# Performance work log

Measured on AMD Instinct MI355X. Metric: run time of the kernel, lower is better.

## Reference

```python
import jax, jax.numpy as jnp
import numpy as np

N = 50000   # nodes
E = 800000  # edges (avg degree 16)
D = 128     # in_feats == out_feats


def setup_inputs() -> dict:
    key = jax.random.key(0)
    k1, k2, k3, k4 = jax.random.split(key, 4)
    h = jax.random.normal(k1, (N, D), dtype=jnp.float32)
    src = jax.random.randint(k2, (E,), 0, N, dtype=jnp.int32)
    dst = jax.random.randint(k3, (E,), 0, N, dtype=jnp.int32)
    snorm_n = jnp.ones((N, 1), dtype=jnp.float32)  # sqrt(1/N) replicated; identity-scaled here
    # NodeApply linear: Linear(2*D, D) with bias
    W = jax.random.normal(k4, (D, 2 * D), dtype=jnp.float32) / np.sqrt(2 * D).astype(np.float32)
    b = jnp.zeros((D,), dtype=jnp.float32)
    return {"h": h, "snorm_n": snorm_n, "W": W, "b": b, "src": src, "dst": dst}


def reference(h, snorm_n, W, b, src, dst):
    # dropout p=0.0 -> identity
    h_in = h
    # gather neighbor messages and segment-mean aggregate (MeanAggregator)
    ones = jnp.ones((src.shape[0],), dtype=h.dtype)
    deg = jax.ops.segment_sum(ones, dst, num_segments=N)            # [N]
    msg_sum = jax.ops.segment_sum(h[src], dst, num_segments=N)     # [N, D]
    c = msg_sum / jnp.maximum(deg, 1.0)[:, None]                   # zero-degree nodes -> c = 0
    # NodeApply: concat -> linear -> L2 normalize -> relu
    bundle = jnp.concatenate([h, c], axis=1) @ W.T + b             # [N, D]
    nrm = jnp.sqrt(jnp.sum(bundle * bundle, axis=1, keepdims=True))
    bundle = bundle / jnp.maximum(nrm, 1e-12)                      # F.normalize(p=2, dim=1)
    out = jax.nn.relu(bundle)
    # graph norm
    out = out * snorm_n
    # residual (in_feats == out_feats)
    return h_in + out
```

## Files before the change

### kernel.cpp

```cpp
#include <hip/hip_runtime.h>
#include <hip/hip_bf16.h>

#define TPB 256
#define CHUNK_LOG 13
#define CHUNK (1 << CHUNK_LOG)
#define HSTRIDE 12544

typedef __attribute__((ext_vector_type(8))) short bf16x8;
typedef __attribute__((ext_vector_type(4))) float f32x4;

__device__ inline unsigned short f2bf(float f) {
    unsigned u = __float_as_uint(f);
    unsigned r = u + 0x7fffu + ((u >> 16) & 1u);
    return (unsigned short)(r >> 16);
}
__device__ inline float bf2f(unsigned short s) {
    return __uint_as_float(((unsigned)s) << 16);
}

__global__ void k_conv(const float* __restrict__ h, const float* __restrict__ W,
                       unsigned short* __restrict__ h_hi,
                       unsigned short* __restrict__ Wb, int N) {
    int t = blockIdx.x * TPB + threadIdx.x;
    int nh4 = N * 32;
    if (t < nh4) {
        float4 v = ((const float4*)h)[t];
        ushort4 hi;
        hi.x = f2bf(v.x); hi.y = f2bf(v.y);
        hi.z = f2bf(v.z); hi.w = f2bf(v.w);
        ((ushort4*)h_hi)[t] = hi;
    } else if (t - nh4 < 8192) {
        int w4 = t - nh4;
        float4 v = ((const float4*)W)[w4];
        ushort4 hi;
        hi.x = f2bf(v.x); hi.y = f2bf(v.y);
        hi.z = f2bf(v.z); hi.w = f2bf(v.w);
        ((ushort4*)Wb)[w4] = hi;
    }
}

__global__ void k_hist(const int* __restrict__ dst,
                       unsigned* __restrict__ hist32, unsigned char* __restrict__ lrank,
                       int E) {
    __shared__ unsigned lhist[HSTRIDE];
    int b = blockIdx.x;
    for (int i = threadIdx.x; i < HSTRIDE; i += TPB) lhist[i] = 0;
    __syncthreads();
    int e0 = b << CHUNK_LOG;
    int e1 = min(e0 + CHUNK, E);
    for (int e = e0 + (int)threadIdx.x; e < e1; e += TPB) {
        int d = dst[e];
        unsigned sh = (d & 3) * 8;
        unsigned old = atomicAdd(&lhist[d >> 2], 1u << sh);
        lrank[e] = (unsigned char)((old >> sh) & 0xffu);
    }
    __syncthreads();
    for (int i = threadIdx.x; i < HSTRIDE; i += TPB)
        hist32[(size_t)b * HSTRIDE + i] = lhist[i];
}

__global__ void k_colscan(const unsigned* __restrict__ hist32,
                          unsigned short* __restrict__ cbase, int* __restrict__ deg,
                          int* __restrict__ bsum, int N, int NBH) {
    extern __shared__ unsigned tile[];
    __shared__ int sdata[4];
    int tileBase = blockIdx.x * 64;
    int total = NBH * 64;
    for (int i = threadIdx.x; i < total; i += TPB) {
        int b = i >> 6, c = i & 63;
        tile[i] = hist32[(size_t)b * HSTRIDE + tileBase + c];
    }
    __syncthreads();
    int t = threadIdx.x;
    int n = blockIdx.x * TPB + t;
    unsigned sh = (t & 3) * 8;
    int wcol = t >> 2;
    int run = 0;
    for (int b = 0; b < NBH; ++b) {
        int c = (int)((tile[b * 64 + wcol] >> sh) & 0xffu);
        if (n < N) cbase[(size_t)b * N + n] = (unsigned short)run;
        run += c;
    }
    if (n < N) deg[n] = run; else run = 0;
    int s = run;
    for (int o = 32; o; o >>= 1) s += __shfl_xor(s, o);
    int lane = t & 63, w = t >> 6;
    if (lane == 0) sdata[w] = s;
    __syncthreads();
    if (t == 0) bsum[blockIdx.x] = sdata[0] + sdata[1] + sdata[2] + sdata[3];
}

__global__ void k_offs2(const int* __restrict__ deg, const int* __restrict__ bsum,
                        int* __restrict__ offs, int N, int E) {
    __shared__ int sb[TPB];
    __shared__ int wsum[4];
    int NB = gridDim.x;
    int t = threadIdx.x;
    int lane = t & 63, w = t >> 6;
    int v = (t < NB) ? bsum[t] : 0;
    int x = v;
    for (int o = 1; o < 64; o <<= 1) { int y = __shfl_up(x, o); if (lane >= o) x += y; }
    if (lane == 63) wsum[w] = x;
    __syncthreads();
    int add = 0;
    for (int k = 0; k < w; ++k) add += wsum[k];
    sb[t] = add + x - v;
    __syncthreads();
    int base = sb[blockIdx.x];
    int i = blockIdx.x * TPB + t;
    int dv = (i < N) ? deg[i] : 0;
    int y2 = dv;
    for (int o = 1; o < 64; o <<= 1) { int z = __shfl_up(y2, o); if (lane >= o) y2 += z; }
    __syncthreads();
    if (lane == 63) wsum[w] = y2;
    __syncthreads();
    int add2 = 0;
    for (int k = 0; k < w; ++k) add2 += wsum[k];
    int ex = base + add2 + y2 - dv;
    if (i < N) offs[i] = ex;
    if (i == N - 1) offs[N] = E;
}

__global__ void k_scatter(const int* __restrict__ src, const int* __restrict__ dst,
                          const unsigned char* __restrict__ lrank,
                          const unsigned short* __restrict__ cbase,
                          const int* __restrict__ offs,
                          unsigned short* __restrict__ esrc, int N, int E, int nchunk) {
    int slice = blockIdx.x & 7;
    int chunk = blockIdx.x >> 3;
    int lo = (int)((long long)N * slice >> 3);
    int hi = (int)((long long)N * (slice + 1) >> 3);
    for (int e = chunk * TPB + threadIdx.x; e < E; e += nchunk * TPB) {
        int d = dst[e];
        if (d >= lo && d < hi) {
            int b = e >> CHUNK_LOG;
            int pos = offs[d] + (int)cbase[(size_t)b * N + d] + (int)lrank[e];
            esrc[pos] = (unsigned short)src[e];
        }
    }
}

__global__ void k_agg(const unsigned short* __restrict__ h_hi, const int* __restrict__ offs,
                      const unsigned short* __restrict__ esrc,
                      unsigned* __restrict__ c, int N) {
    int wid = (blockIdx.x * TPB + threadIdx.x) >> 6;
    int lane = threadIdx.x & 63;
    if (wid >= N) return;
    int beg = offs[wid], end = offs[wid + 1];
    const unsigned* h2 = (const unsigned*)h_hi;
    float ax0 = 0.f, ay0 = 0.f, ax1 = 0.f, ay1 = 0.f;
    int e = beg;
    for (; e + 3 < end; e += 4) {
        int s0 = esrc[e], s1 = esrc[e + 1], s2 = esrc[e + 2], s3 = esrc[e + 3];
        unsigned u0 = h2[(size_t)s0 * 64 + lane];
        unsigned u1 = h2[(size_t)s1 * 64 + lane];
        unsigned u2 = h2[(size_t)s2 * 64 + lane];
        unsigned u3 = h2[(size_t)s3 * 64 + lane];
        ax0 += __uint_as_float(u0 << 16) + __uint_as_float(u1 << 16);
        ay0 += __uint_as_float(u0 & 0xffff0000u) + __uint_as_float(u1 & 0xffff0000u);
        ax1 += __uint_as_float(u2 << 16) + __uint_as_float(u3 << 16);
        ay1 += __uint_as_float(u2 & 0xffff0000u) + __uint_as_float(u3 & 0xffff0000u);
    }
    for (; e < end; ++e) {
        unsigned u0 = h2[(size_t)esrc[e] * 64 + lane];
        ax0 += __uint_as_float(u0 << 16);
        ay0 += __uint_as_float(u0 & 0xffff0000u);
    }
    float ax = ax0 + ax1, ay = ay0 + ay1;
    float inv = 1.0f / fmaxf((float)(end - beg), 1.0f);
    unsigned pk = ((unsigned)f2bf(ay * inv) << 16) | (unsigned)f2bf(ax * inv);
    c[(size_t)wid * 64 + lane] = pk;
}

__launch_bounds__(TPB)
__global__ void k_apply(const unsigned short* __restrict__ h_hi,
                        const unsigned short* __restrict__ c,
                        const unsigned short* __restrict__ Wb,
                        const float* __restrict__ bia,
                        const float* __restrict__ snorm,
                        float* __restrict__ out, int N) {
    int lane = threadIdx.x & 63;
    int l15 = lane & 15, l4 = lane >> 4;
    int wave = threadIdx.x >> 6;
    int r0 = blockIdx.x * 128 + wave * 32;

    f32x4 acc[2][8] = {};

    #pragma unroll
    for (int kc = 0; kc < 8; ++kc) {
        bf16x8 Bf[8];
        #pragma unroll
        for (int n = 0; n < 8; ++n) {
            Bf[n] = *(const bf16x8*)((const char*)Wb +
                     ((size_t)(n * 16 + l15) * 512 + (size_t)kc * 64 + (size_t)l4 * 16));
        }
        #pragma unroll
        for (int rf = 0; rf < 2; ++rf) {
            int row = r0 + rf * 16 + l15;
            if (row > N - 1) row = N - 1;
            bf16x8 av;
            if (kc < 4) {
                av = *(const bf16x8*)((const char*)h_hi +
                      ((size_t)row * 256 + (size_t)kc * 64 + (size_t)l4 * 16));
            } else {
                av = *(const bf16x8*)((const char*)c +
                      ((size_t)row * 256 + (size_t)(kc - 4) * 64 + (size_t)l4 * 16));
            }
            #pragma unroll
            for (int n = 0; n < 8; ++n)
                acc[rf][n] = __builtin_amdgcn_mfma_f32_16x16x32_bf16(av, Bf[n], acc[rf][n], 0, 0, 0);
        }
    }

    float bn[8];
    #pragma unroll
    for (int n = 0; n < 8; ++n) bn[n] = bia[n * 16 + l15];

    #pragma unroll
    for (int rf = 0; rf < 2; ++rf) {
        float sq[4] = {0.f, 0.f, 0.f, 0.f};
        #pragma unroll
        for (int n = 0; n < 8; ++n) {
            #pragma unroll
            for (int g = 0; g < 4; ++g) {
                acc[rf][n][g] += bn[n];
                sq[g] += acc[rf][n][g] * acc[rf][n][g];
            }
        }
        #pragma unroll
        for (int g = 0; g < 4; ++g) {
            sq[g] += __shfl_xor(sq[g], 1);
            sq[g] += __shfl_xor(sq[g], 2);
            sq[g] += __shfl_xor(sq[g], 4);
            sq[g] += __shfl_xor(sq[g], 8);
        }
        #pragma unroll
        for (int g = 0; g < 4; ++g) {
            int row = r0 + rf * 16 + l4 * 4 + g;
            if (row < N) {
                float invn = 1.0f / fmaxf(sqrtf(sq[g]), 1e-12f);
                float sn = snorm[row];
                #pragma unroll
                for (int n = 0; n < 8; ++n) {
                    int col = n * 16 + l15;
                    float res = bf2f(h_hi[(size_t)row * 128 + col]);
                    out[(size_t)row * 128 + col] =
                        fmaxf(acc[rf][n][g] * invn, 0.f) * sn + res;
                }
            }
        }
    }
}

extern "C" void kernel_launch(void* const* d_in, const int* in_sizes, int n_in,
                              void* d_out, int out_size, void* d_ws, size_t ws_size,
                              hipStream_t stream) {
    const float* h     = (const float*)d_in[0];
    const float* snorm = (const float*)d_in[1];
    const float* W     = (const float*)d_in[2];
    const float* b     = (const float*)d_in[3];
    const int*   src   = (const int*)d_in[4];
    const int*   dst   = (const int*)d_in[5];
    int N = in_sizes[1];
    int E = in_sizes[4];
    float* out = (float*)d_out;

    char* ws = (char*)d_ws;
    size_t off = 0;
    auto alloc = [&](size_t bytes) {
        void* ptr = ws + off;
        off = (off + bytes + 255) & ~(size_t)255;
        return ptr;
    };
    int NB  = (N + TPB - 1) / TPB;
    int NBH = (E + CHUNK - 1) >> CHUNK_LOG;
    int* deg    = (int*)alloc((size_t)N * 4);
    int* offs   = (int*)alloc((size_t)(N + 1) * 4);
    int* bsum   = (int*)alloc((size_t)NB * 4);
    unsigned* hist32       = (unsigned*)alloc((size_t)NBH * HSTRIDE * 4);
    unsigned short* cbase  = (unsigned short*)alloc((size_t)NBH * N * 2);
    unsigned char*  lrank  = (unsigned char*)alloc((size_t)E);
    unsigned short* esrc   = (unsigned short*)alloc((size_t)E * 2);
    unsigned short* h_hi   = (unsigned short*)alloc((size_t)N * 128 * 2);
    unsigned short* Wb     = (unsigned short*)alloc((size_t)128 * 256 * 2);
    unsigned* c = hist32;

    int conv_blocks = (N * 32 + 8192 + TPB - 1) / TPB;
    k_conv<<<conv_blocks, TPB, 0, stream>>>(h, W, h_hi, Wb, N);

    k_hist<<<NBH, TPB, 0, stream>>>(dst, hist32, lrank, E);

    size_t tile_bytes = (size_t)NBH * 64 * 4;
    k_colscan<<<NB, TPB, tile_bytes, stream>>>(hist32, cbase, deg, bsum, N, NBH);
    k_offs2<<<NB, TPB, 0, stream>>>(deg, bsum, offs, N, E);

    int nchunk = 512;
    k_scatter<<<8 * nchunk, TPB, 0, stream>>>(src, dst, lrank, cbase, offs, esrc, N, E, nchunk);

    k_agg<<<((size_t)N * 64 + TPB - 1) / TPB, TPB, 0, stream>>>(h_hi, offs, esrc, c, N);

    int nblk = (N + 127) / 128;
    k_apply<<<nblk, TPB, 0, stream>>>(h_hi, (const unsigned short*)c, Wb, b, snorm, out, N);
}
```

Baseline: 114.1 us.

## Gather neighbor features in fp8 and fuse column scan with offsets via grid barrier

The conversion kernel now also writes an fp8 (e4m3) copy of h. The aggregation kernel gathers 2 bytes per lane instead of 4 from that copy, halving random-gather traffic. Separately, the column-scan and offset kernels are merged into one kernel that uses a global atomic counter as a grid-wide barrier to exchange block sums, removing a launch and the deg buffer. The fp8 gather lowers accuracy of the mean, and the spin barrier relies on all 196 blocks being co-resident.

```diff
diff --git a/kernel.cpp b/kernel.cpp
--- a/kernel.cpp
+++ b/kernel.cpp
@@ -8,6 +8,7 @@
 
 typedef __attribute__((ext_vector_type(8))) short bf16x8;
 typedef __attribute__((ext_vector_type(4))) float f32x4;
+typedef __attribute__((ext_vector_type(2))) float f32x2;
 
 __device__ inline unsigned short f2bf(float f) {
     unsigned u = __float_as_uint(f);
@@ -19,8 +20,9 @@
 }
 
 __global__ void k_conv(const float* __restrict__ h, const float* __restrict__ W,
-                       unsigned short* __restrict__ h_hi,
-                       unsigned short* __restrict__ Wb, int N) {
+                       unsigned short* __restrict__ h_hi, unsigned* __restrict__ h8,
+                       unsigned short* __restrict__ Wb, unsigned* ctr, int N) {
+    if (blockIdx.x == 0 && threadIdx.x == 0) *ctr = 0u;
     int t = blockIdx.x * TPB + threadIdx.x;
     int nh4 = N * 32;
     if (t < nh4) {
@@ -29,6 +31,9 @@
         hi.x = f2bf(v.x); hi.y = f2bf(v.y);
         hi.z = f2bf(v.z); hi.w = f2bf(v.w);
         ((ushort4*)h_hi)[t] = hi;
+        int p8 = __builtin_amdgcn_cvt_pk_fp8_f32(v.x, v.y, 0, false);
+        p8 = __builtin_amdgcn_cvt_pk_fp8_f32(v.z, v.w, p8, true);
+        h8[t] = (unsigned)p8;
     } else if (t - nh4 < 8192) {
         int w4 = t - nh4;
         float4 v = ((const float4*)W)[w4];
@@ -59,56 +64,64 @@
         hist32[(size_t)b * HSTRIDE + i] = lhist[i];
 }
 
-__global__ void k_colscan(const unsigned* __restrict__ hist32,
-                          unsigned short* __restrict__ cbase, int* __restrict__ deg,
-                          int* __restrict__ bsum, int N, int NBH) {
+__launch_bounds__(TPB)
+__global__ void k_scan(const unsigned* __restrict__ hist32,
+                       unsigned short* __restrict__ cbase,
+                       int* __restrict__ bsum, unsigned* ctr,
+                       int* __restrict__ offs, int N, int E, int NBH) {
     extern __shared__ unsigned tile[];
     __shared__ int sdata[4];
-    int tileBase = blockIdx.x * 64;
+    __shared__ int sb[TPB];
+    __shared__ int wsum[4];
+    int NB = gridDim.x;
+    int bid = blockIdx.x, tid = threadIdx.x;
+    int lane = tid & 63, w = tid >> 6;
+
+    int tileBase = bid * 64;
     int total = NBH * 64;
-    for (int i = threadIdx.x; i < total; i += TPB) {
+    for (int i = tid; i < total; i += TPB) {
         int b = i >> 6, c = i & 63;
         tile[i] = hist32[(size_t)b * HSTRIDE + tileBase + c];
     }
     __syncthreads();
-    int t = threadIdx.x;
-    int n = blockIdx.x * TPB + t;
-    unsigned sh = (t & 3) * 8;
-    int wcol = t >> 2;
+    int n = bid * TPB + tid;
+    unsigned sh = (tid & 3) * 8;
+    int wcol = tid >> 2;
     int run = 0;
     for (int b = 0; b < NBH; ++b) {
         int c = (int)((tile[b * 64 + wcol] >> sh) & 0xffu);
         if (n < N) cbase[(size_t)b * N + n] = (unsigned short)run;
         run += c;
     }
-    if (n < N) deg[n] = run; else run = 0;
-    int s = run;
+    int dv = (n < N) ? run : 0;
+
+    int s = dv;
     for (int o = 32; o; o >>= 1) s += __shfl_xor(s, o);
-    int lane = t & 63, w = t >> 6;
     if (lane == 0) sdata[w] = s;
     __syncthreads();
-    if (t == 0) bsum[blockIdx.x] = sdata[0] + sdata[1] + sdata[2] + sdata[3];
-}
-
-__global__ void k_offs2(const int* __restrict__ deg, const int* __restrict__ bsum,
-                        int* __restrict__ offs, int N, int E) {
-    __shared__ int sb[TPB];
-    __shared__ int wsum[4];
-    int NB = gridDim.x;
-    int t = threadIdx.x;
-    int lane = t & 63, w = t >> 6;
-    int v = (t < NB) ? bsum[t] : 0;
+    if (tid == 0) {
+        int tot = sdata[0] + sdata[1] + sdata[2] + sdata[3];
+        __hip_atomic_store(&bsum[bid], tot, __ATOMIC_RELAXED, __HIP_MEMORY_SCOPE_AGENT);
+        __hip_atomic_fetch_add(ctr, 1u, __ATOMIC_RELEASE, __HIP_MEMORY_SCOPE_AGENT);
+        while (__hip_atomic_load(ctr, __ATOMIC_ACQUIRE, __HIP_MEMORY_SCOPE_AGENT)
+               < (unsigned)NB)
+            __builtin_amdgcn_s_sleep(2);
+    }
+    __syncthreads();
+
+    int v = 0;
+    if (tid < NB)
+        v = __hip_atomic_load(&bsum[tid], __ATOMIC_RELAXED, __HIP_MEMORY_SCOPE_AGENT);
     int x = v;
     for (int o = 1; o < 64; o <<= 1) { int y = __shfl_up(x, o); if (lane >= o) x += y; }
     if (lane == 63) wsum[w] = x;
     __syncthreads();
     int add = 0;
     for (int k = 0; k < w; ++k) add += wsum[k];
-    sb[t] = add + x - v;
-    __syncthreads();
-    int base = sb[blockIdx.x];
-    int i = blockIdx.x * TPB + t;
-    int dv = (i < N) ? deg[i] : 0;
+    sb[tid] = add + x - v;
+    __syncthreads();
+    int base = sb[bid];
+
     int y2 = dv;
     for (int o = 1; o < 64; o <<= 1) { int z = __shfl_up(y2, o); if (lane >= o) y2 += z; }
     __syncthreads();
@@ -117,8 +130,8 @@
     int add2 = 0;
     for (int k = 0; k < w; ++k) add2 += wsum[k];
     int ex = base + add2 + y2 - dv;
-    if (i < N) offs[i] = ex;
-    if (i == N - 1) offs[N] = E;
+    if (n < N) offs[n] = ex;
+    if (n == N - 1) offs[N] = E;
 }
 
 __global__ void k_scatter(const int* __restrict__ src, const int* __restrict__ dst,
@@ -140,31 +153,32 @@
     }
 }
 
-__global__ void k_agg(const unsigned short* __restrict__ h_hi, const int* __restrict__ offs,
+__global__ void k_agg(const unsigned short* __restrict__ h8s, const int* __restrict__ offs,
                       const unsigned short* __restrict__ esrc,
                       unsigned* __restrict__ c, int N) {
     int wid = (blockIdx.x * TPB + threadIdx.x) >> 6;
     int lane = threadIdx.x & 63;
     if (wid >= N) return;
     int beg = offs[wid], end = offs[wid + 1];
-    const unsigned* h2 = (const unsigned*)h_hi;
     float ax0 = 0.f, ay0 = 0.f, ax1 = 0.f, ay1 = 0.f;
     int e = beg;
     for (; e + 3 < end; e += 4) {
         int s0 = esrc[e], s1 = esrc[e + 1], s2 = esrc[e + 2], s3 = esrc[e + 3];
-        unsigned u0 = h2[(size_t)s0 * 64 + lane];
-        unsigned u1 = h2[(size_t)s1 * 64 + lane];
-        unsigned u2 = h2[(size_t)s2 * 64 + lane];
-        unsigned u3 = h2[(size_t)s3 * 64 + lane];
-        ax0 += __uint_as_float(u0 << 16) + __uint_as_float(u1 << 16);
-        ay0 += __uint_as_float(u0 & 0xffff0000u) + __uint_as_float(u1 & 0xffff0000u);
-        ax1 += __uint_as_float(u2 << 16) + __uint_as_float(u3 << 16);
-        ay1 += __uint_as_float(u2 & 0xffff0000u) + __uint_as_float(u3 & 0xffff0000u);
+        int a0 = h8s[(size_t)s0 * 64 + lane];
+        int a1 = h8s[(size_t)s1 * 64 + lane];
+        int a2 = h8s[(size_t)s2 * 64 + lane];
+        int a3 = h8s[(size_t)s3 * 64 + lane];
+        f32x2 f0 = __builtin_amdgcn_cvt_pk_f32_fp8(a0, false);
+        f32x2 f1 = __builtin_amdgcn_cvt_pk_f32_fp8(a1, false);
+        f32x2 f2 = __builtin_amdgcn_cvt_pk_f32_fp8(a2, false);
+        f32x2 f3 = __builtin_amdgcn_cvt_pk_f32_fp8(a3, false);
+        ax0 += f0.x + f1.x; ay0 += f0.y + f1.y;
+        ax1 += f2.x + f3.x; ay1 += f2.y + f3.y;
     }
     for (; e < end; ++e) {
-        unsigned u0 = h2[(size_t)esrc[e] * 64 + lane];
-        ax0 += __uint_as_float(u0 << 16);
-        ay0 += __uint_as_float(u0 & 0xffff0000u);
+        int a0 = h8s[(size_t)esrc[e] * 64 + lane];
+        f32x2 f0 = __builtin_amdgcn_cvt_pk_f32_fp8(a0, false);
+        ax0 += f0.x; ay0 += f0.y;
     }
     float ax = ax0 + ax1, ay = ay0 + ay1;
     float inv = 1.0f / fmaxf((float)(end - beg), 1.0f);
@@ -274,30 +288,31 @@
     };
     int NB  = (N + TPB - 1) / TPB;
     int NBH = (E + CHUNK - 1) >> CHUNK_LOG;
-    int* deg    = (int*)alloc((size_t)N * 4);
     int* offs   = (int*)alloc((size_t)(N + 1) * 4);
     int* bsum   = (int*)alloc((size_t)NB * 4);
+    unsigned* ctr          = (unsigned*)alloc(256);
     unsigned* hist32       = (unsigned*)alloc((size_t)NBH * HSTRIDE * 4);
     unsigned short* cbase  = (unsigned short*)alloc((size_t)NBH * N * 2);
     unsigned char*  lrank  = (unsigned char*)alloc((size_t)E);
     unsigned short* esrc   = (unsigned short*)alloc((size_t)E * 2);
     unsigned short* h_hi   = (unsigned short*)alloc((size_t)N * 128 * 2);
+    unsigned*       h8     = (unsigned*)alloc((size_t)N * 128);
     unsigned short* Wb     = (unsigned short*)alloc((size_t)128 * 256 * 2);
     unsigned* c = hist32;
 
     int conv_blocks = (N * 32 + 8192 + TPB - 1) / TPB;
-    k_conv<<<conv_blocks, TPB, 0, stream>>>(h, W, h_hi, Wb, N);
+    k_conv<<<conv_blocks, TPB, 0, stream>>>(h, W, h_hi, h8, Wb, ctr, N);
 
     k_hist<<<NBH, TPB, 0, stream>>>(dst, hist32, lrank, E);
 
     size_t tile_bytes = (size_t)NBH * 64 * 4;
-    k_colscan<<<NB, TPB, tile_bytes, stream>>>(hist32, cbase, deg, bsum, N, NBH);
-    k_offs2<<<NB, TPB, 0, stream>>>(deg, bsum, offs, N, E);
+    k_scan<<<NB, TPB, tile_bytes, stream>>>(hist32, cbase, bsum, ctr, offs, N, E, NBH);
 
     int nchunk = 512;
     k_scatter<<<8 * nchunk, TPB, 0, stream>>>(src, dst, lrank, cbase, offs, esrc, N, E, nchunk);
 
-    k_agg<<<((size_t)N * 64 + TPB - 1) / TPB, TPB, 0, stream>>>(h_hi, offs, esrc, c, N);
+    k_agg<<<((size_t)N * 64 + TPB - 1) / TPB, TPB, 0, stream>>>((const unsigned short*)h8,
+                                                                offs, esrc, c, N);
 
     int nblk = (N + 127) / 128;
     k_apply<<<nblk, TPB, 0, stream>>>(h_hi, (const unsigned short*)c, Wb, b, snorm, out, N);
```

After: 116.5 us. 2.1% more time.
